# Kernel tuning notes

Hardware: AMD Instinct MI355X
Metric: run time of the kernel (lower is better)

Reference implementation:

```python
import jax, jax.numpy as jnp
import numpy as np

L, B, N, D, H, DH, M = 2, 8, 1024, 256, 4, 64, 512
EPS = 1e-5


def setup_inputs() -> dict:
    key = jax.random.key(0)
    ks = jax.random.split(key, 24)
    n = lambda k, shape, s=0.02: jax.random.normal(k, shape, dtype=jnp.float32) * s
    return {
        "x": jax.random.normal(ks[0], (B, N, D), dtype=jnp.float32),
        "ln1_g": jnp.ones((L, D), jnp.float32), "ln1_b": jnp.zeros((L, D), jnp.float32),
        "w_qkv": n(ks[1], (L, D, 3 * H * DH)),
        "w_out": n(ks[2], (L, H * DH, D)), "b_out": jnp.zeros((L, D), jnp.float32),
        "ln2_g": jnp.ones((L, D), jnp.float32), "ln2_b": jnp.zeros((L, D), jnp.float32),
        "w_fc1": n(ks[3], (L, D, M)), "b_fc1": jnp.zeros((L, M), jnp.float32),
        "wh": n(ks[4], (L, M, 3), 0.3), "bh": jnp.zeros((L, M), jnp.float32),
        "wv": n(ks[5], (L, M, 3), 0.3), "bv": jnp.zeros((L, M), jnp.float32),
        "bn_g": jnp.ones((L, M), jnp.float32), "bn_b": jnp.zeros((L, M), jnp.float32),
        "bn_m": n(ks[6], (L, M), 0.1),
        "bn_v": jax.random.uniform(ks[7], (L, M), jnp.float32, 0.5, 1.5),
        "w_fc2": n(ks[8], (L, M, D)), "b_fc2": jnp.zeros((L, D), jnp.float32),
        "ls_w1": n(ks[9], (L, D, D // 4)), "ls_w2": n(ks[10], (L, D // 4, D)),
    }


def _ln(z, g, b):
    mu = z.mean(-1, keepdims=True)
    var = ((z - mu) ** 2).mean(-1, keepdims=True)
    return (z - mu) / jnp.sqrt(var + EPS) * g + b


def _lsrc(z, w1, w2):
    # SE gate: global mean over tokens -> FC -> ReLU -> FC -> sigmoid -> scale
    s = jax.nn.sigmoid(jax.nn.relu(z.mean(1) @ w1) @ w2)  # [B, D]
    return z * s[:, None, :]


def reference(x, ln1_g, ln1_b, w_qkv, w_out, b_out, ln2_g, ln2_b, w_fc1, b_fc1,
              wh, bh, wv, bv, bn_g, bn_b, bn_m, bn_v, w_fc2, b_fc2, ls_w1, ls_w2):
    scale = DH ** -0.5
    for l in range(L):
        # --- MHSA (pre-LN) ---
        h = _ln(x, ln1_g[l], ln1_b[l])
        qkv = h @ w_qkv[l]                                  # [B,N,3*H*DH]
        q, k, v = jnp.split(qkv, 3, axis=-1)
        split = lambda t: t.reshape(B, N, H, DH).transpose(0, 2, 1, 3)  # [B,H,N,DH]
        q, k, v = split(q), split(k), split(v)
        attn = jax.nn.softmax(jnp.einsum('bhid,bhjd->bhij', q, k) * scale, axis=-1)
        o = jnp.einsum('bhij,bhjd->bhid', attn, v)
        o = o.transpose(0, 2, 1, 3).reshape(B, N, H * DH)
        y = o @ w_out[l] + b_out[l]                          # dropout = identity (eval)
        x = _lsrc(x + y, ls_w1[l], ls_w2[l])
        # --- MLP with ACB depthwise conv over the token axis ---
        y = jax.nn.gelu(_ln(x, ln2_g[l], ln2_b[l]) @ w_fc1[l] + b_fc1[l], approximate=False)
        # conv_h: depthwise 1x3 conv along N (zero pad)
        yp = jnp.pad(y, ((0, 0), (1, 1), (0, 0)))
        ch = wh[l, :, 0] * yp[:, :-2] + wh[l, :, 1] * yp[:, 1:-1] + wh[l, :, 2] * yp[:, 2:] + bh[l]
        # conv_v: 3x1 depthwise conv on height-1 input with pad 1 -> only center tap
        cv = wv[l, :, 1] * y + bv[l]
        z = ch + cv
        z = (z - bn_m[l]) / jnp.sqrt(bn_v[l] + EPS) * bn_g[l] + bn_b[l]  # BN (eval)
        z = jax.nn.gelu(z, approximate=False)
        y = z @ w_fc2[l] + b_fc2[l]
        x = _lsrc(x + y, ls_w1[l], ls_w2[l])
    return x
```

## Files before the change

kernel.cpp:

```cpp
#include <hip/hip_runtime.h>
#include <hip/hip_bf16.h>
#include <math.h>

#define EPSF 1e-5f

typedef short bf16x8 __attribute__((ext_vector_type(8)));
typedef float f32x4  __attribute__((ext_vector_type(4)));

#define S_BARRIER   __asm__ volatile("s_barrier" ::: "memory")
#define S_WAITV(n)  __asm__ volatile("s_waitcnt vmcnt(" #n ")" ::: "memory")
#define S_WAITL0    __asm__ volatile("s_waitcnt lgkmcnt(0)" ::: "memory")

__device__ __forceinline__ float gelu_f(float z){
  return 0.5f*z*(1.0f + erff(z*0.70710678118654752f));
}
__device__ __forceinline__ unsigned short f2bf(float f){
  unsigned u = __float_as_uint(f);
  u += 0x7FFFu + ((u >> 16) & 1u);
  return (unsigned short)(u >> 16);
}
__device__ __forceinline__ float bf2f(unsigned short u){
  return __uint_as_float((unsigned)u << 16);
}
__device__ __forceinline__ void gll16(const unsigned short* g, unsigned short* l){
  __builtin_amdgcn_global_load_lds(
    (const __attribute__((address_space(1))) unsigned int*)g,
    (__attribute__((address_space(3))) unsigned int*)l, 16, 0, 0);
}

__global__ void tcast_all_k(const float* __restrict__ wqkv, const float* __restrict__ wout,
                            const float* __restrict__ wfc1, const float* __restrict__ wfc2,
                            unsigned short* __restrict__ oqkv, unsigned short* __restrict__ oout,
                            unsigned short* __restrict__ ofc1, unsigned short* __restrict__ ofc2,
                            const float* __restrict__ wh, const float* __restrict__ bh,
                            const float* __restrict__ wv, const float* __restrict__ bv,
                            const float* __restrict__ g, const float* __restrict__ bb,
                            const float* __restrict__ mm, const float* __restrict__ vv,
                            float* __restrict__ cp, float* __restrict__ cm){
  const int b = blockIdx.x, t = threadIdx.x;
  if (b < 256){
    __shared__ unsigned short lt[64*68];
    const int l = b >> 7, r = b & 127;
    const float* in; unsigned short* out; int K, N, tk, tn;
    if (r < 48)      { in=wqkv+(long)l*196608; out=oqkv+(long)l*196608; K=256; N=768; tk=r&3;          tn=r>>2; }
    else if (r < 64) { int q=r-48; in=wout+(long)l*65536;  out=oout+(long)l*65536;  K=256; N=256; tk=q&3; tn=q>>2; }
    else if (r < 96) { int q=r-64; in=wfc1+(long)l*131072; out=ofc1+(long)l*131072; K=256; N=512; tk=q&3; tn=q>>2; }
    else             { int q=r-96; in=wfc2+(long)l*131072; out=ofc2+(long)l*131072; K=512; N=256; tk=q&7; tn=q>>3; }
    const int k0 = tk<<6, n0 = tn<<6;
    const int nn = t & 63, kq = t >> 6;
    #pragma unroll
    for (int i=0;i<16;i++){
      const int kl = kq*16 + i;
      lt[nn*68 + kl] = f2bf(in[(long)(k0+kl)*N + n0 + nn]);
    }
    __syncthreads();
    const int k4 = (t & 15) << 2;
    #pragma unroll
    for (int p=0;p<4;p++){
      const int nl = p*16 + (t>>4);
      *reinterpret_cast<ushort4*>(&out[(long)(n0+nl)*K + k0 + k4]) =
        *reinterpret_cast<const ushort4*>(&lt[nl*68 + k4]);
    }
  } else if (b < 260){
    const int j2 = (b-256)*256 + t;
    const int l = j2 >> 9, j = j2 & 511;
    const int o = l*512 + j;
    float sc = g[o]*rsqrtf(vv[o] + EPSF);
    float* c = cp + (long)l*6*512;
    c[0*512+j] = wh[o*3+0];
    c[1*512+j] = wh[o*3+1] + wv[o*3+1];
    c[2*512+j] = wh[o*3+2];
    c[3*512+j] = bh[o] + bv[o];
    c[4*512+j] = sc;
    c[5*512+j] = bb[o] - mm[o]*sc;
  } else {
    cm[(b-260)*256 + t] = 0.f;
  }
}

__global__ void ln_bf_k(const float* __restrict__ x, const float* __restrict__ g,
                        const float* __restrict__ b, unsigned short* __restrict__ out){
  const int wv = threadIdx.x >> 6, lane = threadIdx.x & 63;
  const int row = blockIdx.x*4 + wv;
  const int c4 = lane*4;
  float4 v = *reinterpret_cast<const float4*>(x + (long)row*256 + c4);
  float s  = v.x+v.y+v.z+v.w;
  float s2 = v.x*v.x+v.y*v.y+v.z*v.z+v.w*v.w;
  #pragma unroll
  for (int o=32;o>0;o>>=1){ s += __shfl_xor(s,o); s2 += __shfl_xor(s2,o); }
  const float mu = s*(1.f/256.f);
  const float rstd = rsqrtf(s2*(1.f/256.f) - mu*mu + EPSF);
  float4 gg = *reinterpret_cast<const float4*>(g + c4);
  float4 bb = *reinterpret_cast<const float4*>(b + c4);
  ushort4 u;
  u.x = f2bf((v.x-mu)*rstd*gg.x + bb.x);
  u.y = f2bf((v.y-mu)*rstd*gg.y + bb.y);
  u.z = f2bf((v.z-mu)*rstd*gg.z + bb.z);
  u.w = f2bf((v.w-mu)*rstd*gg.w + bb.w);
  *reinterpret_cast<ushort4*>(out + (long)row*256 + c4) = u;
}

__global__ void seapply_ln_k(float* __restrict__ x, const float* __restrict__ gate,
                             const float* __restrict__ g, const float* __restrict__ b,
                             unsigned short* __restrict__ out){
  const int wv = threadIdx.x >> 6, lane = threadIdx.x & 63;
  const int row = blockIdx.x*4 + wv;
  const int bi = row >> 10;
  const int c4 = lane*4;
  float4 v = *reinterpret_cast<const float4*>(x + (long)row*256 + c4);
  float4 gt = *reinterpret_cast<const float4*>(gate + bi*256 + c4);
  v.x*=gt.x; v.y*=gt.y; v.z*=gt.z; v.w*=gt.w;
  *reinterpret_cast<float4*>(x + (long)row*256 + c4) = v;
  float s  = v.x+v.y+v.z+v.w;
  float s2 = v.x*v.x+v.y*v.y+v.z*v.z+v.w*v.w;
  #pragma unroll
  for (int o=32;o>0;o>>=1){ s += __shfl_xor(s,o); s2 += __shfl_xor(s2,o); }
  const float mu = s*(1.f/256.f);
  const float rstd = rsqrtf(s2*(1.f/256.f) - mu*mu + EPSF);
  float4 gg = *reinterpret_cast<const float4*>(g + c4);
  float4 bb = *reinterpret_cast<const float4*>(b + c4);
  ushort4 u;
  u.x = f2bf((v.x-mu)*rstd*gg.x + bb.x);
  u.y = f2bf((v.y-mu)*rstd*gg.y + bb.y);
  u.z = f2bf((v.z-mu)*rstd*gg.z + bb.z);
  u.w = f2bf((v.w-mu)*rstd*gg.w + bb.w);
  *reinterpret_cast<ushort4*>(out + (long)row*256 + c4) = u;
}

__global__ void seapply_out_k(const float* __restrict__ x, const float* __restrict__ gate,
                              float* __restrict__ o){
  long o4 = ((long)blockIdx.x*256 + threadIdx.x)*4;
  float4 v = *reinterpret_cast<const float4*>(x+o4);
  float4 g = *reinterpret_cast<const float4*>(gate + (((o4>>18)<<8) | (o4 & 255)));
  v.x*=g.x; v.y*=g.y; v.z*=g.z; v.w*=g.w;
  *reinterpret_cast<float4*>(o+o4) = v;
}

template<int ACT, bool RES, bool BIAS, int OUT, int BMT, int BNT, bool CS>
__global__ __launch_bounds__(256,2)
void gmm_k(const unsigned short* __restrict__ A,
           const unsigned short* __restrict__ Bt,
           void* __restrict__ Cv, int ldc,
           const float* __restrict__ bias,
           const float* __restrict__ res,
           int K, unsigned short* __restrict__ vtb,
           float* __restrict__ cm)
{
  __shared__ unsigned short As[2][BMT*64];
  __shared__ unsigned short Bs[2][BNT*64];
  float* C = (float*)Cv;
  unsigned short* Cb = (unsigned short*)Cv;
  const int tid  = threadIdx.x;
  const int wave = tid>>6, lane = tid&63;
  constexpr int NI = BMT/32;
  constexpr int NJ = BNT/32;
  constexpr int NDMA = BMT/32 + BNT/32;
  const int wm = (wave>>1)*(16*NI), wn = (wave&1)*(BNT/2);
  const int m0 = blockIdx.y*BMT, n0 = blockIdx.x*BNT;
  const int lrow = lane&15, quad = lane>>4;

  f32x4 acc[NI][NJ];
  #pragma unroll
  for (int i=0;i<NI;i++)
    #pragma unroll
    for (int j=0;j<NJ;j++)
      #pragma unroll
      for (int r=0;r<4;r++) acc[i][j][r]=0.f;

  auto stage = [&](int kt, int buf){
    const int k0 = kt<<6;
    #pragma unroll
    for (int it2=0; it2<BMT/32; it2++){
      int idx = tid + it2*256;
      int row = idx>>3, c = idx&7;
      gll16(A + (long)(m0+row)*K + k0 + c*8, &As[buf][idx*8]);
    }
    #pragma unroll
    for (int it2=0; it2<BNT/32; it2++){
      int idx = tid + it2*256;
      int row = idx>>3, c = idx&7;
      gll16(Bt + (long)(n0+row)*K + k0 + c*8, &Bs[buf][idx*8]);
    }
  };

  const int iters = K >> 6;
  stage(0, 0);

  for (int it=0; it<iters; it++){
    const int cur = it & 1;
    if (it+1 < iters){
      stage(it+1, cur^1);
      if constexpr (NDMA==8) { S_WAITV(8); }
      else if constexpr (NDMA==6) { S_WAITV(6); }
      else { S_WAITV(4); }
    } else {
      S_WAITV(0);
    }
    S_BARRIER;

    #pragma unroll
    for (int s=0;s<2;s++){
      bf16x8 a[NI], b[NJ];
      const int ck = s*4 + quad;
      #pragma unroll
      for (int i=0;i<NI;i++)
        a[i] = *reinterpret_cast<const bf16x8*>(&As[cur][(wm+16*i+lrow)*64 + ck*8]);
      #pragma unroll
      for (int j=0;j<NJ;j++)
        b[j] = *reinterpret_cast<const bf16x8*>(&Bs[cur][(wn+16*j+lrow)*64 + ck*8]);
      #pragma unroll
      for (int i=0;i<NI;i++)
        #pragma unroll
        for (int j=0;j<NJ;j++)
          acc[i][j] = __builtin_amdgcn_mfma_f32_16x16x32_bf16(a[i], b[j], acc[i][j], 0,0,0);
    }
    S_WAITL0;
    S_BARRIER;
  }

  if constexpr (OUT==2){
    if (n0 >= 512){
      unsigned short* lt = (unsigned short*)&As[0][0];
      #pragma unroll
      for (int i=0;i<NI;i++){
        const int row_l0 = wm + 16*i + quad*4;
        #pragma unroll
        for (int j=0;j<NJ;j++){
          const int col_l = wn + 16*j + lrow;
          #pragma unroll
          for (int r=0;r<4;r++){
            const int row_l = row_l0 + r;
            lt[col_l*128 + (((row_l>>3) ^ (col_l&7))<<3) + (row_l&7)] = f2bf(acc[i][j][r]);
          }
        }
      }
      __syncthreads();
      const int bb = m0 >> 10, nn0 = m0 & 1023;
      #pragma unroll
      for (int it2=0; it2<8; it2++){
        int idx = tid + it2*256;
        int col_l = idx >> 4;
        int row8 = (idx & 15) << 3;
        uint4 v = *reinterpret_cast<const uint4*>(&lt[col_l*128 + (((row8>>3) ^ (col_l&7))<<3)]);
        int col = n0 + col_l;
        int h = (col-512) >> 6, d = (col-512) & 63;
        *reinterpret_cast<uint4*>(&vtb[(long)((bb*4+h)*64 + d)*1024 + nn0 + row8]) = v;
      }
      return;
    }
    #pragma unroll
    for (int i=0;i<NI;i++){
      const int row0 = m0 + wm + 16*i + quad*4;
      #pragma unroll
      for (int j=0;j<NJ;j++){
        const int col = n0 + wn + 16*j + lrow;
        #pragma unroll
        for (int r=0;r<4;r++)
          Cb[(long)(row0+r)*512 + col] = f2bf(acc[i][j][r]);
      }
    }
    return;
  }

  float csum[NJ];
  #pragma unroll
  for (int j=0;j<NJ;j++) csum[j] = 0.f;

  #pragma unroll
  for (int i=0;i<NI;i++){
    const int row0 = m0 + wm + 16*i + quad*4;
    #pragma unroll
    for (int j=0;j<NJ;j++){
      const int col = n0 + wn + 16*j + lrow;
      const float bv = BIAS ? bias[col] : 0.f;
      #pragma unroll
      for (int r=0;r<4;r++){
        const long off = (long)(row0+r)*ldc + col;
        float v = acc[i][j][r] + bv;
        if (RES) v += res[off];
        if (ACT==1) v = gelu_f(v);
        if (CS) csum[j] += v;
        if (OUT==1) Cb[off] = f2bf(v); else C[off] = v;
      }
    }
  }
  if (CS){
    float* red = (float*)&As[0][0];
    for (int j = tid; j < BNT; j += 256) red[j] = 0.f;
    __syncthreads();
    #pragma unroll
    for (int j=0;j<NJ;j++)
      atomicAdd(&red[wn + 16*j + lrow], csum[j]);
    __syncthreads();
    const int bb = m0 >> 10;
    for (int j = tid; j < BNT; j += 256)
      atomicAdd(&cm[bb*256 + n0 + j], red[j]);
  }
}

__global__ __launch_bounds__(256)
void attn_k(const unsigned short* __restrict__ qkb,
            const unsigned short* __restrict__ vtb,
            unsigned short* __restrict__ o){
  const int q0 = blockIdx.x * 64;
  const int bh = blockIdx.y;
  const int b = bh >> 2, h = bh & 3;
  const int tid = threadIdx.x;
  const int wv = tid >> 6;
  const int lane = tid & 63;
  const int l15 = lane & 15, quad = lane >> 4;

  __shared__ unsigned short Qs[64*64];
  __shared__ unsigned short Ks[64*64];
  __shared__ unsigned short Vt[64*64];
  __shared__ unsigned short Ps[64*64];

  const long rowbase = (long)b*1024;
  const unsigned short* vsrc = vtb + (long)bh*64*1024;

  for (int f = tid; f < 512; f += 256){
    int row = f >> 3, g = f & 7;
    *reinterpret_cast<uint4*>(&Qs[row*64 + (g ^ (row&7))*8]) =
      *reinterpret_cast<const uint4*>(qkb + (rowbase + q0 + row)*512 + h*64 + g*8);
  }

  const int row0 = tid >> 3, g0 = tid & 7;
  const int row1 = row0 + 32;
  uint4 kr0, vr0, kr1, vr1;
  auto pre = [&](int k0){
    kr0 = *reinterpret_cast<const uint4*>(qkb + (rowbase + k0 + row0)*512 + 256 + h*64 + g0*8);
    vr0 = *reinterpret_cast<const uint4*>(vsrc + (long)row0*1024 + k0 + g0*8);
    kr1 = *reinterpret_cast<const uint4*>(qkb + (rowbase + k0 + row1)*512 + 256 + h*64 + g0*8);
    vr1 = *reinterpret_cast<const uint4*>(vsrc + (long)row1*1024 + k0 + g0*8);
  };

  float lp[4];
  f32x4 acc[4];
  #pragma unroll
  for (int r=0;r<4;r++) lp[r] = 0.f;
  #pragma unroll
  for (int j=0;j<4;j++)
    #pragma unroll
    for (int r=0;r<4;r++) acc[j][r] = 0.f;

  pre(0);
  for (int k0 = 0; k0 < 1024; k0 += 64){
    *reinterpret_cast<uint4*>(&Ks[row0*64 + (g0 ^ (row0&7))*8]) = kr0;
    *reinterpret_cast<uint4*>(&Vt[row0*64 + (g0 ^ (row0&7))*8]) = vr0;
    *reinterpret_cast<uint4*>(&Ks[row1*64 + (g0 ^ (row1&7))*8]) = kr1;
    *reinterpret_cast<uint4*>(&Vt[row1*64 + (g0 ^ (row1&7))*8]) = vr1;
    __syncthreads();
    if (k0 + 64 < 1024) pre(k0 + 64);

    f32x4 s[4];
    #pragma unroll
    for (int j=0;j<4;j++)
      #pragma unroll
      for (int r=0;r<4;r++) s[j][r] = 0.f;

    #pragma unroll
    for (int half=0; half<2; half++){
      const int ck = half*4 + quad;
      const int qrow = 16*wv + l15;
      bf16x8 a = *reinterpret_cast<const bf16x8*>(&Qs[qrow*64 + (ck ^ (qrow&7))*8]);
      #pragma unroll
      for (int j=0;j<4;j++){
        int krow = 16*j + l15;
        bf16x8 bb = *reinterpret_cast<const bf16x8*>(&Ks[krow*64 + (ck ^ (krow&7))*8]);
        s[j] = __builtin_amdgcn_mfma_f32_16x16x32_bf16(a, bb, s[j], 0,0,0);
      }
    }

    #pragma unroll
    for (int r=0;r<4;r++)
      #pragma unroll
      for (int j=0;j<4;j++){
        float p = __expf(s[j][r]*0.125f);
        s[j][r] = p;
        lp[r] += p;
      }

    #pragma unroll
    for (int j=0;j<4;j++)
      #pragma unroll
      for (int r=0;r<4;r++){
        int rowq = 16*wv + quad*4 + r;
        int key = l15 + 16*j;
        Ps[rowq*64 + (((key>>3) ^ ((rowq>>2)&7)))*8 + (key&7)] = f2bf(s[j][r]);
      }

    #pragma unroll
    for (int half=0; half<2; half++){
      const int ck = half*4 + quad;
      const int prow = 16*wv + l15;
      bf16x8 a = *reinterpret_cast<const bf16x8*>(&Ps[prow*64 + (ck ^ ((prow>>2)&7))*8]);
      #pragma unroll
      for (int jj=0;jj<4;jj++){
        int drow = 16*jj + l15;
        bf16x8 bb = *reinterpret_cast<const bf16x8*>(&Vt[drow*64 + (ck ^ (drow&7))*8]);
        acc[jj] = __builtin_amdgcn_mfma_f32_16x16x32_bf16(a, bb, acc[jj], 0,0,0);
      }
    }
    __syncthreads();
  }

  #pragma unroll
  for (int r=0;r<4;r++){
    float l = lp[r];
    l += __shfl_xor(l, 1); l += __shfl_xor(l, 2);
    l += __shfl_xor(l, 4); l += __shfl_xor(l, 8);
    const float inv = 1.f / l;
    const int rloc = q0 + 16*wv + quad*4 + r;
    const long grow = rowbase + rloc;
    #pragma unroll
    for (int jj=0;jj<4;jj++)
      o[grow*256 + h*64 + 16*jj + l15] = f2bf(acc[jj][r]*inv);
  }
}

__global__ void segate2_k(float* __restrict__ cm, const float* __restrict__ w1,
                          const float* __restrict__ w2, float* __restrict__ gate){
  const int b = blockIdx.x, t = threadIdx.x;
  __shared__ float sc[256], sh[64];
  sc[t] = cm[b*256+t]*(1.f/1024.f);
  cm[b*256+t] = 0.f;
  __syncthreads();
  {
    const int j = t >> 2, part = t & 3;
    float a = 0.f;
    #pragma unroll 4
    for (int i=0;i<64;i++){
      const int k = i*4 + part;
      a += sc[k]*w1[k*64+j];
    }
    a += __shfl_xor(a, 1);
    a += __shfl_xor(a, 2);
    if (part == 0) sh[j] = fmaxf(a, 0.f);
  }
  __syncthreads();
  float a = 0.f;
  #pragma unroll 8
  for (int k=0;k<64;k++) a += sh[k]*w2[k*256+t];
  gate[b*256+t] = 1.f/(1.f+__expf(-a));
}

__global__ void conv_bf_k(const unsigned short* __restrict__ y, unsigned short* __restrict__ z,
                          const float* __restrict__ cp)
{
  const int t = threadIdx.x;
  const int rr = t >> 6;
  const int row = blockIdx.x*4 + rr;
  const int n = row & 1023;
  const int c8 = (t & 63) * 8;
  const long base = (long)row*512 + c8;

  uint4 uc = *reinterpret_cast<const uint4*>(y + base);
  uint4 um = (n>0)    ? *reinterpret_cast<const uint4*>(y + base - 512) : uint4{0,0,0,0};
  uint4 up = (n<1023) ? *reinterpret_cast<const uint4*>(y + base + 512) : uint4{0,0,0,0};
  const unsigned short* yc = reinterpret_cast<const unsigned short*>(&uc);
  const unsigned short* ym = reinterpret_cast<const unsigned short*>(&um);
  const unsigned short* yp = reinterpret_cast<const unsigned short*>(&up);

  float c0[8], c1[8], c2[8], c3[8], s5[8], b5[8];
  #pragma unroll
  for (int q=0;q<8;q+=4){
    *reinterpret_cast<float4*>(&c0[q]) = *reinterpret_cast<const float4*>(cp + 0*512 + c8 + q);
    *reinterpret_cast<float4*>(&c1[q]) = *reinterpret_cast<const float4*>(cp + 1*512 + c8 + q);
    *reinterpret_cast<float4*>(&c2[q]) = *reinterpret_cast<const float4*>(cp + 2*512 + c8 + q);
    *reinterpret_cast<float4*>(&c3[q]) = *reinterpret_cast<const float4*>(cp + 3*512 + c8 + q);
    *reinterpret_cast<float4*>(&s5[q]) = *reinterpret_cast<const float4*>(cp + 4*512 + c8 + q);
    *reinterpret_cast<float4*>(&b5[q]) = *reinterpret_cast<const float4*>(cp + 5*512 + c8 + q);
  }

  unsigned short outv[8];
  #pragma unroll
  for (int q=0;q<8;q++){
    float zz = c0[q]*bf2f(ym[q]) + c1[q]*bf2f(yc[q]) + c2[q]*bf2f(yp[q]) + c3[q];
    zz = zz*s5[q] + b5[q];
    outv[q] = f2bf(gelu_f(zz));
  }
  *reinterpret_cast<uint4*>(z + base) = *reinterpret_cast<uint4*>(outv);
}

extern "C" void kernel_launch(void* const* d_in, const int* in_sizes, int n_in,
                              void* d_out, int out_size, void* d_ws, size_t ws_size,
                              hipStream_t stream)
{
  const float* x_in  = (const float*)d_in[0];
  const float* ln1_g = (const float*)d_in[1];
  const float* ln1_b = (const float*)d_in[2];
  const float* w_qkv = (const float*)d_in[3];
  const float* w_out = (const float*)d_in[4];
  const float* b_out = (const float*)d_in[5];
  const float* ln2_g = (const float*)d_in[6];
  const float* ln2_b = (const float*)d_in[7];
  const float* w_fc1 = (const float*)d_in[8];
  const float* b_fc1 = (const float*)d_in[9];
  const float* wh    = (const float*)d_in[10];
  const float* bh    = (const float*)d_in[11];
  const float* wv    = (const float*)d_in[12];
  const float* bv    = (const float*)d_in[13];
  const float* bn_g  = (const float*)d_in[14];
  const float* bn_b  = (const float*)d_in[15];
  const float* bn_m  = (const float*)d_in[16];
  const float* bn_v  = (const float*)d_in[17];
  const float* w_fc2 = (const float*)d_in[18];
  const float* b_fc2 = (const float*)d_in[19];
  const float* ls_w1 = (const float*)d_in[20];
  const float* ls_w2 = (const float*)d_in[21];

  float* ws   = (float*)d_ws;
  float* xbuf = ws;
  float* cm   = xbuf + 2097152;
  float* gate = cm + 2048;
  float* cpar = gate + 2048;
  unsigned short* habf = (unsigned short*)(cpar + 6144);
  unsigned short* qkb  = habf + 2097152;
  unsigned short* vtb  = qkb  + 4194304;
  unsigned short* ybf  = vtb  + 2097152;
  unsigned short* zbf  = ybf  + 4194304;
  unsigned short* wqkv_t = zbf + 4194304;
  unsigned short* wout_t = wqkv_t + 393216;
  unsigned short* wfc1_t = wout_t + 131072;
  unsigned short* wfc2_t = wfc1_t + 262144;

  tcast_all_k<<<268,256,0,stream>>>(w_qkv, w_out, w_fc1, w_fc2,
                                    wqkv_t, wout_t, wfc1_t, wfc2_t,
                                    wh, bh, wv, bv, bn_g, bn_b, bn_m, bn_v, cpar, cm);

  for (int l=0;l<2;l++){
    const float* bout_l = b_out + l*256;
    const float* bfc1_l = b_fc1 + l*512;
    const float* bfc2_l = b_fc2 + l*256;
    const float* lw1_l  = ls_w1 + (long)l*256*64;
    const float* lw2_l  = ls_w2 + (long)l*64*256;
    const float* resx   = (l==0) ? x_in : xbuf;

    if (l==0)
      ln_bf_k<<<2048,256,0,stream>>>(x_in, ln1_g, ln1_b, habf);
    gmm_k<0,false,false,2,128,128,false><<<dim3(6,64),256,0,stream>>>(
        habf, wqkv_t + (long)l*768*256, (void*)qkb, 512, nullptr, nullptr, 256, vtb, nullptr);
    attn_k<<<dim3(16,32),256,0,stream>>>(qkb, vtb, habf);
    gmm_k<0,true,true,0,64,64,true><<<dim3(4,128),256,0,stream>>>(
        habf, wout_t + (long)l*256*256, (void*)xbuf, 256, bout_l, resx, 256, nullptr, cm);

    segate2_k<<<8,256,0,stream>>>(cm, lw1_l, lw2_l, gate);
    seapply_ln_k<<<2048,256,0,stream>>>(xbuf, gate, ln2_g + l*256, ln2_b + l*256, habf);

    gmm_k<1,false,true,1,128,128,false><<<dim3(4,64),256,0,stream>>>(
        habf, wfc1_t + (long)l*512*256, (void*)ybf, 512, bfc1_l, nullptr, 256, nullptr, nullptr);
    conv_bf_k<<<2048,256,0,stream>>>(ybf, zbf, cpar + (long)l*6*512);
    gmm_k<0,true,true,0,64,64,true><<<dim3(4,128),256,0,stream>>>(
        zbf, wfc2_t + (long)l*256*512, (void*)xbuf, 256, bfc2_l, xbuf, 512, nullptr, cm);

    segate2_k<<<8,256,0,stream>>>(cm, lw1_l, lw2_l, gate);
    if (l==0)
      seapply_ln_k<<<2048,256,0,stream>>>(xbuf, gate, ln1_g + 256, ln1_b + 256, habf);
    else
      seapply_out_k<<<2048,256,0,stream>>>(xbuf, gate, (float*)d_out);
  }
}
```

Before: 317.5 us.

## Fuse SE gate into GEMM epilogue, LN into prep, split-K attention

The SE gate computation moves into the residual GEMM epilogue: the last block per batch, found with an atomic counter, computes the gate, which removes the separate segate2 launches. The first LayerNorm is folded into the weight-cast prep kernel to save a launch. Attention now uses 32-query tiles with 128-key tiles split across wave pairs, merged through shared memory, and Q stays in registers. The softmax scale is folded into the QKV epilogue. This adds threadfence and atomic counter overhead, and the unshifted exp, kept from before, still carries overflow risk.

```diff
diff --git a/kernel.cpp b/kernel.cpp
--- a/kernel.cpp
+++ b/kernel.cpp
@@ -36,7 +36,10 @@
                             const float* __restrict__ wv, const float* __restrict__ bv,
                             const float* __restrict__ g, const float* __restrict__ bb,
                             const float* __restrict__ mm, const float* __restrict__ vv,
-                            float* __restrict__ cp, float* __restrict__ cm){
+                            float* __restrict__ cp, float* __restrict__ cm,
+                            int* __restrict__ cnt,
+                            const float* __restrict__ x, const float* __restrict__ lg,
+                            const float* __restrict__ lb, unsigned short* __restrict__ lnout){
   const int b = blockIdx.x, t = threadIdx.x;
   if (b < 256){
     __shared__ unsigned short lt[64*68];
@@ -73,31 +76,30 @@
     c[3*512+j] = bh[o] + bv[o];
     c[4*512+j] = sc;
     c[5*512+j] = bb[o] - mm[o]*sc;
+  } else if (b < 268){
+    cm[(b-260)*256 + t] = 0.f;
+  } else if (b == 268){
+    if (t < 16) cnt[t] = 0;
   } else {
-    cm[(b-260)*256 + t] = 0.f;
-  }
-}
-
-__global__ void ln_bf_k(const float* __restrict__ x, const float* __restrict__ g,
-                        const float* __restrict__ b, unsigned short* __restrict__ out){
-  const int wv = threadIdx.x >> 6, lane = threadIdx.x & 63;
-  const int row = blockIdx.x*4 + wv;
-  const int c4 = lane*4;
-  float4 v = *reinterpret_cast<const float4*>(x + (long)row*256 + c4);
-  float s  = v.x+v.y+v.z+v.w;
-  float s2 = v.x*v.x+v.y*v.y+v.z*v.z+v.w*v.w;
-  #pragma unroll
-  for (int o=32;o>0;o>>=1){ s += __shfl_xor(s,o); s2 += __shfl_xor(s2,o); }
-  const float mu = s*(1.f/256.f);
-  const float rstd = rsqrtf(s2*(1.f/256.f) - mu*mu + EPSF);
-  float4 gg = *reinterpret_cast<const float4*>(g + c4);
-  float4 bb = *reinterpret_cast<const float4*>(b + c4);
-  ushort4 u;
-  u.x = f2bf((v.x-mu)*rstd*gg.x + bb.x);
-  u.y = f2bf((v.y-mu)*rstd*gg.y + bb.y);
-  u.z = f2bf((v.z-mu)*rstd*gg.z + bb.z);
-  u.w = f2bf((v.w-mu)*rstd*gg.w + bb.w);
-  *reinterpret_cast<ushort4*>(out + (long)row*256 + c4) = u;
+    const int wv2 = t >> 6, lane = t & 63;
+    const int row = (b-269)*4 + wv2;
+    const int c4 = lane*4;
+    float4 v = *reinterpret_cast<const float4*>(x + (long)row*256 + c4);
+    float s  = v.x+v.y+v.z+v.w;
+    float s2 = v.x*v.x+v.y*v.y+v.z*v.z+v.w*v.w;
+    #pragma unroll
+    for (int o=32;o>0;o>>=1){ s += __shfl_xor(s,o); s2 += __shfl_xor(s2,o); }
+    const float mu = s*(1.f/256.f);
+    const float rstd = rsqrtf(s2*(1.f/256.f) - mu*mu + EPSF);
+    float4 gg = *reinterpret_cast<const float4*>(lg + c4);
+    float4 bv2 = *reinterpret_cast<const float4*>(lb + c4);
+    ushort4 u;
+    u.x = f2bf((v.x-mu)*rstd*gg.x + bv2.x);
+    u.y = f2bf((v.y-mu)*rstd*gg.y + bv2.y);
+    u.z = f2bf((v.z-mu)*rstd*gg.z + bv2.z);
+    u.w = f2bf((v.w-mu)*rstd*gg.w + bv2.w);
+    *reinterpret_cast<ushort4*>(lnout + (long)row*256 + c4) = u;
+  }
 }
 
 __global__ void seapply_ln_k(float* __restrict__ x, const float* __restrict__ gate,
@@ -144,7 +146,9 @@
            const float* __restrict__ bias,
            const float* __restrict__ res,
            int K, unsigned short* __restrict__ vtb,
-           float* __restrict__ cm)
+           float* __restrict__ cm,
+           const float* __restrict__ w1, const float* __restrict__ w2,
+           float* __restrict__ gate, int* __restrict__ cnt)
 {
   __shared__ unsigned short As[2][BMT*64];
   __shared__ unsigned short Bs[2][BNT*64];
@@ -248,6 +252,7 @@
       }
       return;
     }
+    const float qs = (n0 < 256) ? 0.125f : 1.f;
     #pragma unroll
     for (int i=0;i<NI;i++){
       const int row0 = m0 + wm + 16*i + quad*4;
@@ -256,7 +261,7 @@
         const int col = n0 + wn + 16*j + lrow;
         #pragma unroll
         for (int r=0;r<4;r++)
-          Cb[(long)(row0+r)*512 + col] = f2bf(acc[i][j][r]);
+          Cb[(long)(row0+r)*512 + col] = f2bf(acc[i][j][r]*qs);
       }
     }
     return;
@@ -295,6 +300,37 @@
     const int bb = m0 >> 10;
     for (int j = tid; j < BNT; j += 256)
       atomicAdd(&cm[bb*256 + n0 + j], red[j]);
+
+    __threadfence();
+    __shared__ int lastf;
+    if (tid==0) lastf = (atomicAdd(&cnt[bb], 1) == 63) ? 1 : 0;
+    __syncthreads();
+    if (lastf){
+      float* sc = (float*)&Bs[0][0];
+      float* sh = sc + 256;
+      float v = __hip_atomic_load(&cm[bb*256+tid], __ATOMIC_RELAXED, __HIP_MEMORY_SCOPE_AGENT);
+      sc[tid] = v*(1.f/1024.f);
+      cm[bb*256+tid] = 0.f;
+      __syncthreads();
+      {
+        const int j = tid >> 2, part = tid & 3;
+        float a = 0.f;
+        #pragma unroll 4
+        for (int i=0;i<64;i++){
+          const int k = i*4 + part;
+          a += sc[k]*w1[k*64+j];
+        }
+        a += __shfl_xor(a, 1);
+        a += __shfl_xor(a, 2);
+        if (part == 0) sh[j] = fmaxf(a, 0.f);
+      }
+      __syncthreads();
+      float a = 0.f;
+      #pragma unroll 8
+      for (int k=0;k<64;k++) a += sh[k]*w2[k*256+tid];
+      gate[bb*256+tid] = 1.f/(1.f+__expf(-a));
+      if (tid==0) cnt[bb] = 0;
+    }
   }
 }
 
@@ -302,36 +338,43 @@
 void attn_k(const unsigned short* __restrict__ qkb,
             const unsigned short* __restrict__ vtb,
             unsigned short* __restrict__ o){
-  const int q0 = blockIdx.x * 64;
+  const int q0 = blockIdx.x * 32;
   const int bh = blockIdx.y;
   const int b = bh >> 2, h = bh & 3;
   const int tid = threadIdx.x;
   const int wv = tid >> 6;
   const int lane = tid & 63;
   const int l15 = lane & 15, quad = lane >> 4;
-
-  __shared__ unsigned short Qs[64*64];
-  __shared__ unsigned short Ks[64*64];
-  __shared__ unsigned short Vt[64*64];
-  __shared__ unsigned short Ps[64*64];
+  const int wq = wv & 1, kh = wv >> 1;
+
+  __shared__ unsigned short Ks[128*64];
+  __shared__ unsigned short Vt[64*128];
+  __shared__ unsigned short Ps[32*128];
 
   const long rowbase = (long)b*1024;
   const unsigned short* vsrc = vtb + (long)bh*64*1024;
 
-  for (int f = tid; f < 512; f += 256){
-    int row = f >> 3, g = f & 7;
-    *reinterpret_cast<uint4*>(&Qs[row*64 + (g ^ (row&7))*8]) =
-      *reinterpret_cast<const uint4*>(qkb + (rowbase + q0 + row)*512 + h*64 + g*8);
-  }
-
-  const int row0 = tid >> 3, g0 = tid & 7;
-  const int row1 = row0 + 32;
-  uint4 kr0, vr0, kr1, vr1;
+  bf16x8 aq[2];
+  {
+    const int qrow = q0 + 16*wq + l15;
+    #pragma unroll
+    for (int half=0; half<2; half++)
+      aq[half] = *reinterpret_cast<const bf16x8*>(
+          qkb + (rowbase + qrow)*512 + h*64 + (half*4+quad)*8);
+  }
+
+  const int krow_b = tid >> 3, g0 = tid & 7;
+  const int vd = tid >> 4, kg = tid & 15;
+  uint4 kr[4], vr[4];
   auto pre = [&](int k0){
-    kr0 = *reinterpret_cast<const uint4*>(qkb + (rowbase + k0 + row0)*512 + 256 + h*64 + g0*8);
-    vr0 = *reinterpret_cast<const uint4*>(vsrc + (long)row0*1024 + k0 + g0*8);
-    kr1 = *reinterpret_cast<const uint4*>(qkb + (rowbase + k0 + row1)*512 + 256 + h*64 + g0*8);
-    vr1 = *reinterpret_cast<const uint4*>(vsrc + (long)row1*1024 + k0 + g0*8);
+    #pragma unroll
+    for (int i=0;i<4;i++)
+      kr[i] = *reinterpret_cast<const uint4*>(
+          qkb + (rowbase + k0 + krow_b + 32*i)*512 + 256 + h*64 + g0*8);
+    #pragma unroll
+    for (int i=0;i<4;i++)
+      vr[i] = *reinterpret_cast<const uint4*>(
+          vsrc + (long)(vd + 16*i)*1024 + k0 + kg*8);
   };
 
   float lp[4];
@@ -344,13 +387,19 @@
     for (int r=0;r<4;r++) acc[j][r] = 0.f;
 
   pre(0);
-  for (int k0 = 0; k0 < 1024; k0 += 64){
-    *reinterpret_cast<uint4*>(&Ks[row0*64 + (g0 ^ (row0&7))*8]) = kr0;
-    *reinterpret_cast<uint4*>(&Vt[row0*64 + (g0 ^ (row0&7))*8]) = vr0;
-    *reinterpret_cast<uint4*>(&Ks[row1*64 + (g0 ^ (row1&7))*8]) = kr1;
-    *reinterpret_cast<uint4*>(&Vt[row1*64 + (g0 ^ (row1&7))*8]) = vr1;
+  for (int k0 = 0; k0 < 1024; k0 += 128){
+    #pragma unroll
+    for (int i=0;i<4;i++){
+      const int row = krow_b + 32*i;
+      *reinterpret_cast<uint4*>(&Ks[row*64 + ((g0 ^ (row&7))<<3)]) = kr[i];
+    }
+    #pragma unroll
+    for (int i=0;i<4;i++){
+      const int d = vd + 16*i;
+      *reinterpret_cast<uint4*>(&Vt[d*128 + (kg>>3)*64 + (((kg&7) ^ (d&7))<<3)]) = vr[i];
+    }
     __syncthreads();
-    if (k0 + 64 < 1024) pre(k0 + 64);
+    if (k0 + 128 < 1024) pre(k0 + 128);
 
     f32x4 s[4];
     #pragma unroll
@@ -361,13 +410,11 @@
     #pragma unroll
     for (int half=0; half<2; half++){
       const int ck = half*4 + quad;
-      const int qrow = 16*wv + l15;
-      bf16x8 a = *reinterpret_cast<const bf16x8*>(&Qs[qrow*64 + (ck ^ (qrow&7))*8]);
       #pragma unroll
       for (int j=0;j<4;j++){
-        int krow = 16*j + l15;
-        bf16x8 bb = *reinterpret_cast<const bf16x8*>(&Ks[krow*64 + (ck ^ (krow&7))*8]);
-        s[j] = __builtin_amdgcn_mfma_f32_16x16x32_bf16(a, bb, s[j], 0,0,0);
+        const int krow = 64*kh + 16*j + l15;
+        bf16x8 bb = *reinterpret_cast<const bf16x8*>(&Ks[krow*64 + ((ck ^ (krow&7))<<3)]);
+        s[j] = __builtin_amdgcn_mfma_f32_16x16x32_bf16(aq[half], bb, s[j], 0,0,0);
       }
     }
 
@@ -375,7 +422,7 @@
     for (int r=0;r<4;r++)
       #pragma unroll
       for (int j=0;j<4;j++){
-        float p = __expf(s[j][r]*0.125f);
+        float p = __expf(s[j][r]);
         s[j][r] = p;
         lp[r] += p;
       }
@@ -384,64 +431,62 @@
     for (int j=0;j<4;j++)
       #pragma unroll
       for (int r=0;r<4;r++){
-        int rowq = 16*wv + quad*4 + r;
-        int key = l15 + 16*j;
-        Ps[rowq*64 + (((key>>3) ^ ((rowq>>2)&7)))*8 + (key&7)] = f2bf(s[j][r]);
+        const int rowq = 16*wq + quad*4 + r;
+        const int keyl = l15 + 16*j;
+        Ps[rowq*128 + kh*64 + ((((keyl>>3) ^ ((rowq>>2)&7)))<<3) + (keyl&7)] = f2bf(s[j][r]);
       }
 
     #pragma unroll
     for (int half=0; half<2; half++){
       const int ck = half*4 + quad;
-      const int prow = 16*wv + l15;
-      bf16x8 a = *reinterpret_cast<const bf16x8*>(&Ps[prow*64 + (ck ^ ((prow>>2)&7))*8]);
+      const int prow = 16*wq + l15;
+      bf16x8 a = *reinterpret_cast<const bf16x8*>(&Ps[prow*128 + kh*64 + ((ck ^ ((prow>>2)&7))<<3)]);
       #pragma unroll
       for (int jj=0;jj<4;jj++){
-        int drow = 16*jj + l15;
-        bf16x8 bb = *reinterpret_cast<const bf16x8*>(&Vt[drow*64 + (ck ^ (drow&7))*8]);
+        const int drow = 16*jj + l15;
+        bf16x8 bb = *reinterpret_cast<const bf16x8*>(&Vt[drow*128 + kh*64 + ((ck ^ (drow&7))<<3)]);
         acc[jj] = __builtin_amdgcn_mfma_f32_16x16x32_bf16(a, bb, acc[jj], 0,0,0);
       }
     }
     __syncthreads();
   }
 
-  #pragma unroll
-  for (int r=0;r<4;r++){
-    float l = lp[r];
-    l += __shfl_xor(l, 1); l += __shfl_xor(l, 2);
-    l += __shfl_xor(l, 4); l += __shfl_xor(l, 8);
-    const float inv = 1.f / l;
-    const int rloc = q0 + 16*wv + quad*4 + r;
-    const long grow = rowbase + rloc;
+  float* MO  = (float*)Ks;
+  float* MLp = (float*)Vt;
+  if (kh == 1){
     #pragma unroll
     for (int jj=0;jj<4;jj++)
-      o[grow*256 + h*64 + 16*jj + l15] = f2bf(acc[jj][r]*inv);
-  }
-}
-
-__global__ void segate2_k(float* __restrict__ cm, const float* __restrict__ w1,
-                          const float* __restrict__ w2, float* __restrict__ gate){
-  const int b = blockIdx.x, t = threadIdx.x;
-  __shared__ float sc[256], sh[64];
-  sc[t] = cm[b*256+t]*(1.f/1024.f);
-  cm[b*256+t] = 0.f;
+      #pragma unroll
+      for (int r=0;r<4;r++)
+        MO[(wq*64 + lane)*16 + jj*4 + r] = acc[jj][r];
+    #pragma unroll
+    for (int r=0;r<4;r++)
+      MLp[(wq*64 + lane)*4 + r] = lp[r];
+  }
   __syncthreads();
-  {
-    const int j = t >> 2, part = t & 3;
-    float a = 0.f;
-    #pragma unroll 4
-    for (int i=0;i<64;i++){
-      const int k = i*4 + part;
-      a += sc[k]*w1[k*64+j];
-    }
-    a += __shfl_xor(a, 1);
-    a += __shfl_xor(a, 2);
-    if (part == 0) sh[j] = fmaxf(a, 0.f);
-  }
-  __syncthreads();
-  float a = 0.f;
-  #pragma unroll 8
-  for (int k=0;k<64;k++) a += sh[k]*w2[k*256+t];
-  gate[b*256+t] = 1.f/(1.f+__expf(-a));
+  if (kh == 0){
+    #pragma unroll
+    for (int jj=0;jj<4;jj++)
+      #pragma unroll
+      for (int r=0;r<4;r++)
+        acc[jj][r] += MO[(wq*64 + lane)*16 + jj*4 + r];
+    #pragma unroll
+    for (int r=0;r<4;r++)
+      lp[r] += MLp[(wq*64 + lane)*4 + r];
+
+    #pragma unroll
+    for (int r=0;r<4;r++){
+      float l = lp[r];
+      l += __shfl_xor(l, 1); l += __shfl_xor(l, 2);
+      l += __shfl_xor(l, 4); l += __shfl_xor(l, 8);
+      const float inv = 1.f / l;
+      const int rloc = q0 + 16*wq + quad*4 + r;
+      const long grow = rowbase + rloc;
+      #pragma unroll
+      for (int jj=0;jj<4;jj++)
+        o[grow*256 + h*64 + 16*jj + l15] = f2bf(acc[jj][r]*inv);
+    }
+  }
 }
 
 __global__ void conv_bf_k(const unsigned short* __restrict__ y, unsigned short* __restrict__ z,
@@ -514,7 +559,8 @@
   float* cm   = xbuf + 2097152;
   float* gate = cm + 2048;
   float* cpar = gate + 2048;
-  unsigned short* habf = (unsigned short*)(cpar + 6144);
+  int*   cnt  = (int*)(cpar + 6144);
+  unsigned short* habf = (unsigned short*)(cpar + 6144 + 16);
   unsigned short* qkb  = habf + 2097152;
   unsigned short* vtb  = qkb  + 4194304;
   unsigned short* ybf  = vtb  + 2097152;
@@ -524,9 +570,10 @@
   unsigned short* wfc1_t = wout_t + 131072;
   unsigned short* wfc2_t = wfc1_t + 262144;
 
-  tcast_all_k<<<268,256,0,stream>>>(w_qkv, w_out, w_fc1, w_fc2,
-                                    wqkv_t, wout_t, wfc1_t, wfc2_t,
-                                    wh, bh, wv, bv, bn_g, bn_b, bn_m, bn_v, cpar, cm);
+  tcast_all_k<<<2317,256,0,stream>>>(w_qkv, w_out, w_fc1, w_fc2,
+                                     wqkv_t, wout_t, wfc1_t, wfc2_t,
+                                     wh, bh, wv, bv, bn_g, bn_b, bn_m, bn_v, cpar, cm, cnt,
+                                     x_in, ln1_g, ln1_b, habf);
 
   for (int l=0;l<2;l++){
     const float* bout_l = b_out + l*256;
@@ -536,24 +583,24 @@
     const float* lw2_l  = ls_w2 + (long)l*64*256;
     const float* resx   = (l==0) ? x_in : xbuf;
 
-    if (l==0)
-      ln_bf_k<<<2048,256,0,stream>>>(x_in, ln1_g, ln1_b, habf);
     gmm_k<0,false,false,2,128,128,false><<<dim3(6,64),256,0,stream>>>(
-        habf, wqkv_t + (long)l*768*256, (void*)qkb, 512, nullptr, nullptr, 256, vtb, nullptr);
-    attn_k<<<dim3(16,32),256,0,stream>>>(qkb, vtb, habf);
+        habf, wqkv_t + (long)l*768*256, (void*)qkb, 512, nullptr, nullptr, 256, vtb,
+        nullptr, nullptr, nullptr, nullptr, nullptr);
+    attn_k<<<dim3(32,32),256,0,stream>>>(qkb, vtb, habf);
     gmm_k<0,true,true,0,64,64,true><<<dim3(4,128),256,0,stream>>>(
-        habf, wout_t + (long)l*256*256, (void*)xbuf, 256, bout_l, resx, 256, nullptr, cm);
-
-    segate2_k<<<8,256,0,stream>>>(cm, lw1_l, lw2_l, gate);
+        habf, wout_t + (long)l*256*256, (void*)xbuf, 256, bout_l, resx, 256, nullptr,
+        cm, lw1_l, lw2_l, gate, cnt);
+
     seapply_ln_k<<<2048,256,0,stream>>>(xbuf, gate, ln2_g + l*256, ln2_b + l*256, habf);
 
     gmm_k<1,false,true,1,128,128,false><<<dim3(4,64),256,0,stream>>>(
-        habf, wfc1_t + (long)l*512*256, (void*)ybf, 512, bfc1_l, nullptr, 256, nullptr, nullptr);
+        habf, wfc1_t + (long)l*512*256, (void*)ybf, 512, bfc1_l, nullptr, 256, nullptr,
+        nullptr, nullptr, nullptr, nullptr, nullptr);
     conv_bf_k<<<2048,256,0,stream>>>(ybf, zbf, cpar + (long)l*6*512);
     gmm_k<0,true,true,0,64,64,true><<<dim3(4,128),256,0,stream>>>(
-        zbf, wfc2_t + (long)l*256*512, (void*)xbuf, 256, bfc2_l, xbuf, 512, nullptr, cm);
-
-    segate2_k<<<8,256,0,stream>>>(cm, lw1_l, lw2_l, gate);
+        zbf, wfc2_t + (long)l*256*512, (void*)xbuf, 256, bfc2_l, xbuf, 512, nullptr,
+        cm, lw1_l, lw2_l, gate, cnt);
+
     if (l==0)
       seapply_ln_k<<<2048,256,0,stream>>>(xbuf, gate, ln1_g + 256, ln1_b + 256, habf);
     else
```

After: 605.4 us. 90.7% more time.

## Fuse first LayerNorm into prep kernel, swizzle GEMM LDS, fold softmax scale into Q

Applied to the files above, without the earlier changes.

The first-layer LayerNorm is merged into the weight-cast/parameter prep kernel by appending 2048 extra blocks, which removes one launch. The GEMM global-to-LDS loads and the fragment reads now use an XOR swizzle on 16-byte chunks to reduce LDS bank conflicts. The attention scale of 0.125 moves into the QKV GEMM epilogue, applied to the Q columns before the bf16 cast, so the per-element multiply in the attention kernel goes away. Rounding Q after scaling changes bf16 rounding slightly, since a power-of-two scale is exact anyway.

```diff
diff --git a/kernel.cpp b/kernel.cpp
--- a/kernel.cpp
+++ b/kernel.cpp
@@ -36,7 +36,9 @@
                             const float* __restrict__ wv, const float* __restrict__ bv,
                             const float* __restrict__ g, const float* __restrict__ bb,
                             const float* __restrict__ mm, const float* __restrict__ vv,
-                            float* __restrict__ cp, float* __restrict__ cm){
+                            float* __restrict__ cp, float* __restrict__ cm,
+                            const float* __restrict__ x, const float* __restrict__ lg,
+                            const float* __restrict__ lb, unsigned short* __restrict__ lnout){
   const int b = blockIdx.x, t = threadIdx.x;
   if (b < 256){
     __shared__ unsigned short lt[64*68];
@@ -73,31 +75,28 @@
     c[3*512+j] = bh[o] + bv[o];
     c[4*512+j] = sc;
     c[5*512+j] = bb[o] - mm[o]*sc;
+  } else if (b < 268){
+    cm[(b-260)*256 + t] = 0.f;
   } else {
-    cm[(b-260)*256 + t] = 0.f;
-  }
-}
-
-__global__ void ln_bf_k(const float* __restrict__ x, const float* __restrict__ g,
-                        const float* __restrict__ b, unsigned short* __restrict__ out){
-  const int wv = threadIdx.x >> 6, lane = threadIdx.x & 63;
-  const int row = blockIdx.x*4 + wv;
-  const int c4 = lane*4;
-  float4 v = *reinterpret_cast<const float4*>(x + (long)row*256 + c4);
-  float s  = v.x+v.y+v.z+v.w;
-  float s2 = v.x*v.x+v.y*v.y+v.z*v.z+v.w*v.w;
-  #pragma unroll
-  for (int o=32;o>0;o>>=1){ s += __shfl_xor(s,o); s2 += __shfl_xor(s2,o); }
-  const float mu = s*(1.f/256.f);
-  const float rstd = rsqrtf(s2*(1.f/256.f) - mu*mu + EPSF);
-  float4 gg = *reinterpret_cast<const float4*>(g + c4);
-  float4 bb = *reinterpret_cast<const float4*>(b + c4);
-  ushort4 u;
-  u.x = f2bf((v.x-mu)*rstd*gg.x + bb.x);
-  u.y = f2bf((v.y-mu)*rstd*gg.y + bb.y);
-  u.z = f2bf((v.z-mu)*rstd*gg.z + bb.z);
-  u.w = f2bf((v.w-mu)*rstd*gg.w + bb.w);
-  *reinterpret_cast<ushort4*>(out + (long)row*256 + c4) = u;
+    const int wv2 = t >> 6, lane = t & 63;
+    const int row = (b-268)*4 + wv2;
+    const int c4 = lane*4;
+    float4 v = *reinterpret_cast<const float4*>(x + (long)row*256 + c4);
+    float s  = v.x+v.y+v.z+v.w;
+    float s2 = v.x*v.x+v.y*v.y+v.z*v.z+v.w*v.w;
+    #pragma unroll
+    for (int o=32;o>0;o>>=1){ s += __shfl_xor(s,o); s2 += __shfl_xor(s2,o); }
+    const float mu = s*(1.f/256.f);
+    const float rstd = rsqrtf(s2*(1.f/256.f) - mu*mu + EPSF);
+    float4 gg = *reinterpret_cast<const float4*>(lg + c4);
+    float4 bv2 = *reinterpret_cast<const float4*>(lb + c4);
+    ushort4 u;
+    u.x = f2bf((v.x-mu)*rstd*gg.x + bv2.x);
+    u.y = f2bf((v.y-mu)*rstd*gg.y + bv2.y);
+    u.z = f2bf((v.z-mu)*rstd*gg.z + bv2.z);
+    u.w = f2bf((v.w-mu)*rstd*gg.w + bv2.w);
+    *reinterpret_cast<ushort4*>(lnout + (long)row*256 + c4) = u;
+  }
 }
 
 __global__ void seapply_ln_k(float* __restrict__ x, const float* __restrict__ gate,
@@ -158,6 +157,7 @@
   const int wm = (wave>>1)*(16*NI), wn = (wave&1)*(BNT/2);
   const int m0 = blockIdx.y*BMT, n0 = blockIdx.x*BNT;
   const int lrow = lane&15, quad = lane>>4;
+  const int sx = lrow & 7;
 
   f32x4 acc[NI][NJ];
   #pragma unroll
@@ -173,13 +173,13 @@
     for (int it2=0; it2<BMT/32; it2++){
       int idx = tid + it2*256;
       int row = idx>>3, c = idx&7;
-      gll16(A + (long)(m0+row)*K + k0 + c*8, &As[buf][idx*8]);
+      gll16(A + (long)(m0+row)*K + k0 + ((c ^ (row&7))<<3), &As[buf][idx*8]);
     }
     #pragma unroll
     for (int it2=0; it2<BNT/32; it2++){
       int idx = tid + it2*256;
       int row = idx>>3, c = idx&7;
-      gll16(Bt + (long)(n0+row)*K + k0 + c*8, &Bs[buf][idx*8]);
+      gll16(Bt + (long)(n0+row)*K + k0 + ((c ^ (row&7))<<3), &Bs[buf][idx*8]);
     }
   };
 
@@ -202,12 +202,13 @@
     for (int s=0;s<2;s++){
       bf16x8 a[NI], b[NJ];
       const int ck = s*4 + quad;
+      const int cs = (ck ^ sx) << 3;
       #pragma unroll
       for (int i=0;i<NI;i++)
-        a[i] = *reinterpret_cast<const bf16x8*>(&As[cur][(wm+16*i+lrow)*64 + ck*8]);
+        a[i] = *reinterpret_cast<const bf16x8*>(&As[cur][(wm+16*i+lrow)*64 + cs]);
       #pragma unroll
       for (int j=0;j<NJ;j++)
-        b[j] = *reinterpret_cast<const bf16x8*>(&Bs[cur][(wn+16*j+lrow)*64 + ck*8]);
+        b[j] = *reinterpret_cast<const bf16x8*>(&Bs[cur][(wn+16*j+lrow)*64 + cs]);
       #pragma unroll
       for (int i=0;i<NI;i++)
         #pragma unroll
@@ -248,6 +249,7 @@
       }
       return;
     }
+    const float qs = (n0 < 256) ? 0.125f : 1.f;
     #pragma unroll
     for (int i=0;i<NI;i++){
       const int row0 = m0 + wm + 16*i + quad*4;
@@ -256,7 +258,7 @@
         const int col = n0 + wn + 16*j + lrow;
         #pragma unroll
         for (int r=0;r<4;r++)
-          Cb[(long)(row0+r)*512 + col] = f2bf(acc[i][j][r]);
+          Cb[(long)(row0+r)*512 + col] = f2bf(acc[i][j][r]*qs);
       }
     }
     return;
@@ -375,7 +377,7 @@
     for (int r=0;r<4;r++)
       #pragma unroll
       for (int j=0;j<4;j++){
-        float p = __expf(s[j][r]*0.125f);
+        float p = __expf(s[j][r]);
         s[j][r] = p;
         lp[r] += p;
       }
@@ -524,9 +526,10 @@
   unsigned short* wfc1_t = wout_t + 131072;
   unsigned short* wfc2_t = wfc1_t + 262144;
 
-  tcast_all_k<<<268,256,0,stream>>>(w_qkv, w_out, w_fc1, w_fc2,
-                                    wqkv_t, wout_t, wfc1_t, wfc2_t,
-                                    wh, bh, wv, bv, bn_g, bn_b, bn_m, bn_v, cpar, cm);
+  tcast_all_k<<<2316,256,0,stream>>>(w_qkv, w_out, w_fc1, w_fc2,
+                                     wqkv_t, wout_t, wfc1_t, wfc2_t,
+                                     wh, bh, wv, bv, bn_g, bn_b, bn_m, bn_v, cpar, cm,
+                                     x_in, ln1_g, ln1_b, habf);
 
   for (int l=0;l<2;l++){
     const float* bout_l = b_out + l*256;
@@ -536,8 +539,6 @@
     const float* lw2_l  = ls_w2 + (long)l*64*256;
     const float* resx   = (l==0) ? x_in : xbuf;
 
-    if (l==0)
-      ln_bf_k<<<2048,256,0,stream>>>(x_in, ln1_g, ln1_b, habf);
     gmm_k<0,false,false,2,128,128,false><<<dim3(6,64),256,0,stream>>>(
         habf, wqkv_t + (long)l*768*256, (void*)qkb, 512, nullptr, nullptr, 256, vtb, nullptr);
     attn_k<<<dim3(16,32),256,0,stream>>>(qkb, vtb, habf);
```

After: 306.6 us. -3.4%, faster.
